# Kernel optimization log

Hardware: AMD Instinct MI355X
Metric: run time of the kernel (lower is better)

## Reference

```python
import jax, jax.numpy as jnp
import numpy as np

DIM = 256; H = 64; W = 64; NH = 8; NL = 1; NP = 8; HD = DIM // NH
B = 4


def _bilinear(img, grid):
    """torch.grid_sample(mode='bilinear', padding='zeros', align_corners=False).
    img: [C, Hl, Wl]; grid: [N, P, 2] normalized xy in [-1, 1]. Returns [C, N, P]."""
    Hl, Wl = img.shape[1], img.shape[2]
    x = (grid[..., 0] + 1.0) * (Wl * 0.5) - 0.5
    y = (grid[..., 1] + 1.0) * (Hl * 0.5) - 0.5
    x0 = jnp.floor(x); y0 = jnp.floor(y)
    wx = x - x0; wy = y - y0

    def gather(xi, yi):
        valid = (xi >= 0) & (xi < Wl) & (yi >= 0) & (yi < Hl)
        xc = jnp.clip(xi, 0, Wl - 1).astype(jnp.int32)
        yc = jnp.clip(yi, 0, Hl - 1).astype(jnp.int32)
        return img[:, yc, xc] * valid.astype(img.dtype)[None]  # [C, N, P]

    v00 = gather(x0, y0); v01 = gather(x0 + 1, y0)
    v10 = gather(x0, y0 + 1); v11 = gather(x0 + 1, y0 + 1)
    top = v00 * (1.0 - wx) + v01 * wx
    bot = v10 * (1.0 - wx) + v11 * wx
    return top * (1.0 - wy) + bot * wy


def _msda(value, loc, att):
    """multi_scale_deformable_attn_pytorch.
    value: [b, nv, NH, HD]; loc: [b, nq, NH, NL, NP, 2] in [0,1]; att: [b, nq, NH, NL, NP]."""
    b, nv, _, _ = value.shape
    nq = loc.shape[1]
    grids = 2.0 * loc - 1.0
    bn = b * NH
    level_shapes = [(H, W)] * NL  # all levels share the single [H, W] grid here
    sampled_levels = []
    offset = 0
    for l, (Hl, Wl) in enumerate(level_shapes):
        vl = value[:, offset:offset + Hl * Wl]                     # [b, HW, NH, HD]
        offset += Hl * Wl
        vl = vl.transpose(0, 2, 3, 1).reshape(bn, HD, Hl, Wl)      # [b*NH, HD, Hl, Wl]
        gl = grids[:, :, :, l].transpose(0, 2, 1, 3, 4).reshape(bn, nq, NP, 2)
        sampled_levels.append(jax.vmap(_bilinear)(vl, gl))         # [b*NH, HD, nq, NP]
    sampled = jnp.stack(sampled_levels, axis=3)                    # [b*NH, HD, nq, NL, NP]
    w = att.transpose(0, 2, 1, 3, 4).reshape(bn, 1, nq, NL, NP)
    out = jnp.sum(sampled * w, axis=(3, 4))                        # [b*NH, HD, nq]
    return out.reshape(b, NH, HD, nq).transpose(0, 3, 1, 2).reshape(b, nq, NH * HD)


def _forward(query, value, W_loc, b_loc, W_att, b_att, W_val, b_val, W_out, b_out):
    b = query.shape[0]
    nq = H * W
    q = query.transpose(0, 2, 3, 1).reshape(b, nq, DIM)
    v = value.transpose(0, 2, 3, 1).reshape(b, nq, DIM)
    loc = (q @ W_loc.T + b_loc).reshape(b, nq, NH, NL, NP, 2)
    att = jax.nn.softmax((q @ W_att.T + b_att).reshape(b, nq, NH, NL * NP), axis=-1)
    att = att.reshape(b, nq, NH, NL, NP)
    v = (v @ W_val.T + b_val).reshape(b, nq, NH, HD)
    out = _msda(v, loc, att)                                       # [b, nq, DIM]
    return out @ W_out.T + b_out


def setup_inputs() -> dict:
    key = jax.random.key(0)
    ks = jax.random.split(key, 12)
    s = 0.02
    return {
        "query": jax.random.normal(ks[0], (B, DIM, H, W), jnp.float32),
        "value": jax.random.normal(ks[1], (B, DIM, H, W), jnp.float32),
        "W_loc": jax.random.normal(ks[2], (NH * NL * NP * 2, DIM), jnp.float32) * s,
        "b_loc": jax.random.normal(ks[3], (NH * NL * NP * 2,), jnp.float32) * s,
        "W_att": jax.random.normal(ks[4], (NH * NL * NP, DIM), jnp.float32) * s,
        "b_att": jax.random.normal(ks[5], (NH * NL * NP,), jnp.float32) * s,
        "W_val": jax.random.normal(ks[6], (DIM, DIM), jnp.float32) * s,
        "b_val": jax.random.normal(ks[7], (DIM,), jnp.float32) * s,
        "W_out": jax.random.normal(ks[8], (DIM, DIM), jnp.float32) * s,
        "b_out": jax.random.normal(ks[9], (DIM,), jnp.float32) * s,
    }


def reference(query, value, W_loc, b_loc, W_att, b_att, W_val, b_val, W_out, b_out):
    return _forward(query, value, W_loc, b_loc, W_att, b_att, W_val, b_val, W_out, b_out)
```

## Files before the change

kernel.cpp:

```cpp
#include <hip/hip_runtime.h>
#include <hip/hip_bf16.h>
#include <math.h>

#define NQ   4096
#define DIMC 256
#define NHC  8
#define NPC  8
#define HDC  32
#define HC   64
#define WC   64
#define BC   4
#define KSTR 264

typedef __bf16 bf16x8 __attribute__((ext_vector_type(8)));
typedef __attribute__((ext_vector_type(4))) float f4;
typedef __attribute__((ext_vector_type(8))) short s8v;

__device__ __forceinline__ ushort f2bf(float f) {
  __hip_bfloat16 h = __float2bfloat16(f);
  union { __hip_bfloat16 h; ushort u; } c; c.h = h; return c.u;
}
__device__ __forceinline__ float bfu2f(ushort u) {
  union { unsigned i; float f; } c; c.i = ((unsigned)u) << 16; return c.f;
}
__device__ __forceinline__ float bflo(unsigned u) {
  union { unsigned i; float f; } c; c.i = u << 16; return c.f;
}
__device__ __forceinline__ float bfhi(unsigned u) {
  union { unsigned i; float f; } c; c.i = u & 0xffff0000u; return c.f;
}

union bfr8 { ushort u[8]; bf16x8 v; s8v s; };

__global__ __launch_bounds__(256) void k_proj(
    const float* __restrict__ query, const float* __restrict__ value,
    const float* __restrict__ W_loc, const float* __restrict__ b_loc,
    const float* __restrict__ W_att, const float* __restrict__ b_att,
    const float* __restrict__ W_val, const float* __restrict__ b_val,
    float* __restrict__ loc, float* __restrict__ att,
    ushort* __restrict__ vproj) {
  __shared__ __align__(16) ushort smem[2 * 64 * KSTR];
  const int tid = threadIdx.x;
  const int b = blockIdx.z, n0 = blockIdx.x * 64;
  const int lane = tid & 63, wid = tid >> 6;
  const int am = lane & 15, kq = (lane >> 4) * 8;
  const int row4 = (lane >> 4) * 4;
  const int an = tid & 63, ak = (tid >> 6) * 8;

  if (blockIdx.y == 0) {
    ushort* Ah = smem;
    ushort* Al = smem + 64 * KSTR;
    const float* Xb = query + (size_t)b * DIMC * NQ + n0 + an;
    for (int t = 0; t < 8; ++t) {
      const int kb = t * 32 + ak;
      float x[8];
#pragma unroll
      for (int j = 0; j < 8; ++j) x[j] = Xb[(size_t)(kb + j) * NQ];
      bfr8 ph, pl;
#pragma unroll
      for (int j = 0; j < 8; ++j) {
        ushort h = f2bf(x[j]);
        ph.u[j] = h;
        pl.u[j] = f2bf(x[j] - bfu2f(h));
      }
      *(s8v*)(&Ah[an * KSTR + kb]) = ph.s;
      *(s8v*)(&Al[an * KSTR + kb]) = pl.s;
    }
    __syncthreads();

    const int o0w = wid * 48;
    const float* Wr[3];
#pragma unroll
    for (int oj = 0; oj < 3; ++oj) {
      const int o = o0w + oj * 16 + am;
      Wr[oj] = (o < 128) ? (W_loc + (size_t)o * DIMC)
                         : (W_att + (size_t)(o - 128) * DIMC);
    }
    f4 acc[4][3];
#pragma unroll
    for (int mi = 0; mi < 4; ++mi)
#pragma unroll
      for (int oj = 0; oj < 3; ++oj) acc[mi][oj] = (f4)0.f;

#pragma unroll
    for (int t = 0; t < 8; ++t) {
      const int kk = t * 32 + kq;
      bf16x8 ah[4], al[4];
#pragma unroll
      for (int mi = 0; mi < 4; ++mi) {
        ah[mi] = *(const bf16x8*)(&Ah[(mi * 16 + am) * KSTR + kk]);
        al[mi] = *(const bf16x8*)(&Al[(mi * 16 + am) * KSTR + kk]);
      }
#pragma unroll
      for (int oj = 0; oj < 3; ++oj) {
        const float4 w0 = *(const float4*)(Wr[oj] + kk);
        const float4 w1 = *(const float4*)(Wr[oj] + kk + 4);
        const float wt[8] = {w0.x, w0.y, w0.z, w0.w, w1.x, w1.y, w1.z, w1.w};
        bfr8 bh, bl;
#pragma unroll
        for (int j = 0; j < 8; ++j) {
          ushort h = f2bf(wt[j]);
          bh.u[j] = h;
          bl.u[j] = f2bf(wt[j] - bfu2f(h));
        }
#pragma unroll
        for (int mi = 0; mi < 4; ++mi) {
          acc[mi][oj] = __builtin_amdgcn_mfma_f32_16x16x32_bf16(ah[mi], bh.v, acc[mi][oj], 0, 0, 0);
          acc[mi][oj] = __builtin_amdgcn_mfma_f32_16x16x32_bf16(al[mi], bh.v, acc[mi][oj], 0, 0, 0);
          acc[mi][oj] = __builtin_amdgcn_mfma_f32_16x16x32_bf16(ah[mi], bl.v, acc[mi][oj], 0, 0, 0);
        }
      }
    }
#pragma unroll
    for (int oj = 0; oj < 3; ++oj) {
      const int oA = o0w + oj * 16;
      const bool isAtt = (oA >= 128);
      float* dstBase = isAtt ? att : loc;
      const float* bias = isAtt ? b_att : b_loc;
      const int ostride = isAtt ? 64 : 128;
      const int o = (isAtt ? oA - 128 : oA) + am;
      const float bv = bias[o];
#pragma unroll
      for (int mi = 0; mi < 4; ++mi) {
        const int nb = n0 + mi * 16 + row4;
#pragma unroll
        for (int r = 0; r < 4; ++r)
          dstBase[((size_t)b * NQ + nb + r) * ostride + o] = acc[mi][oj][r] + bv;
      }
    }
  } else {
    ushort* As = smem;
    const float* Xb = value + (size_t)b * DIMC * NQ + n0 + an;
    for (int t = 0; t < 8; ++t) {
      const int kb = t * 32 + ak;
      float x[8];
#pragma unroll
      for (int j = 0; j < 8; ++j) x[j] = Xb[(size_t)(kb + j) * NQ];
      bfr8 pa;
#pragma unroll
      for (int j = 0; j < 8; ++j) pa.u[j] = f2bf(x[j]);
      *(s8v*)(&As[an * KSTR + kb]) = pa.s;
    }
    __syncthreads();

    const int o0w = wid * 64;
    const float* Wr[4];
#pragma unroll
    for (int oj = 0; oj < 4; ++oj)
      Wr[oj] = W_val + (size_t)(o0w + oj * 16 + am) * DIMC;

    f4 acc[4][4];
#pragma unroll
    for (int mi = 0; mi < 4; ++mi)
#pragma unroll
      for (int oj = 0; oj < 4; ++oj) acc[mi][oj] = (f4)0.f;

#pragma unroll
    for (int t = 0; t < 8; ++t) {
      const int kk = t * 32 + kq;
      bf16x8 af[4];
#pragma unroll
      for (int mi = 0; mi < 4; ++mi)
        af[mi] = *(const bf16x8*)(&As[(mi * 16 + am) * KSTR + kk]);
#pragma unroll
      for (int oj = 0; oj < 4; ++oj) {
        const float4 w0 = *(const float4*)(Wr[oj] + kk);
        const float4 w1 = *(const float4*)(Wr[oj] + kk + 4);
        const float wt[8] = {w0.x, w0.y, w0.z, w0.w, w1.x, w1.y, w1.z, w1.w};
        bfr8 bh;
#pragma unroll
        for (int j = 0; j < 8; ++j) bh.u[j] = f2bf(wt[j]);
#pragma unroll
        for (int mi = 0; mi < 4; ++mi)
          acc[mi][oj] = __builtin_amdgcn_mfma_f32_16x16x32_bf16(af[mi], bh.v, acc[mi][oj], 0, 0, 0);
      }
    }
#pragma unroll
    for (int oj = 0; oj < 4; ++oj) {
      const int o = o0w + oj * 16 + am;
      const int h = o >> 5, d = o & 31;
      const float bias = b_val[o];
      ushort* dst = vproj + ((size_t)(b * NHC + h) * NQ) * HDC + d;
#pragma unroll
      for (int mi = 0; mi < 4; ++mi) {
        const int nb = n0 + mi * 16 + row4;
#pragma unroll
        for (int r = 0; r < 4; ++r)
          dst[(size_t)(nb + r) * HDC] = f2bf(acc[mi][oj][r] + bias);
      }
    }
  }
}

__global__ __launch_bounds__(256) void k_sample(
    const float* __restrict__ loc, const float* __restrict__ attL,
    const ushort* __restrict__ vproj, ushort* __restrict__ msda) {
  __shared__ float4 Lc[64][9];
  __shared__ int4   Lo[64][9];
  const int b = blockIdx.z, h = blockIdx.y;
  const int tid = threadIdx.x;
  const int n0 = blockIdx.x * 64;
#pragma unroll
  for (int it = 0; it < 2; ++it) {
    const int idx = it * 256 + tid;
    const int q = idx >> 3, p = idx & 7;
    const int n = n0 + q;
    const float lg = attL[((size_t)b * NQ + n) * 64 + h * 8 + p];
    float m = lg;
#pragma unroll
    for (int off = 1; off < 8; off <<= 1) m = fmaxf(m, __shfl_xor(m, off, 64));
    const float e = __expf(lg - m);
    float s = e;
#pragma unroll
    for (int off = 1; off < 8; off <<= 1) s += __shfl_xor(s, off, 64);
    const float w = e / s;
    const float2 xy = *(const float2*)(loc + ((size_t)b * NQ + n) * 128 + h * 16 + p * 2);
    const float x = xy.x * 64.0f - 0.5f;
    const float y = xy.y * 64.0f - 0.5f;
    const float x0f = floorf(x), y0f = floorf(y);
    const float wx = x - x0f, wy = y - y0f;
    const int x0 = (int)x0f, y0 = (int)y0f;
    const int x1 = x0 + 1, y1 = y0 + 1;
    const float fx0 = (x0 >= 0 && x0 < WC) ? 1.f : 0.f;
    const float fx1 = (x1 >= 0 && x1 < WC) ? 1.f : 0.f;
    const float fy0 = (y0 >= 0 && y0 < HC) ? 1.f : 0.f;
    const float fy1 = (y1 >= 0 && y1 < HC) ? 1.f : 0.f;
    const int cx0 = min(max(x0, 0), WC - 1), cx1 = min(max(x1, 0), WC - 1);
    const int cy0 = min(max(y0, 0), HC - 1), cy1 = min(max(y1, 0), HC - 1);
    float4 cf;
    cf.x = w * (1.f - wx) * (1.f - wy) * fx0 * fy0;
    cf.y = w * wx * (1.f - wy) * fx1 * fy0;
    cf.z = w * (1.f - wx) * wy * fx0 * fy1;
    cf.w = w * wx * wy * fx1 * fy1;
    int4 of;
    of.x = (cy0 * WC + cx0) * HDC; of.y = (cy0 * WC + cx1) * HDC;
    of.z = (cy1 * WC + cx0) * HDC; of.w = (cy1 * WC + cx1) * HDC;
    Lc[q][p] = cf; Lo[q][p] = of;
  }
  __syncthreads();
  const int q = tid >> 2, d8 = (tid & 3) * 8;
  const int n = n0 + q;
  const ushort* vb = vproj + (size_t)((b * NHC + h) * NQ) * HDC + d8;
  float a[8] = {};
#pragma unroll
  for (int p = 0; p < 8; ++p) {
    const int4 of = Lo[q][p];
    const float4 cf = Lc[q][p];
    const uint4 u00 = *(const uint4*)(vb + of.x);
    const uint4 u01 = *(const uint4*)(vb + of.y);
    const uint4 u10 = *(const uint4*)(vb + of.z);
    const uint4 u11 = *(const uint4*)(vb + of.w);
    const unsigned c00[4] = {u00.x, u00.y, u00.z, u00.w};
    const unsigned c01[4] = {u01.x, u01.y, u01.z, u01.w};
    const unsigned c10[4] = {u10.x, u10.y, u10.z, u10.w};
    const unsigned c11[4] = {u11.x, u11.y, u11.z, u11.w};
#pragma unroll
    for (int j = 0; j < 4; ++j) {
      a[2 * j]     += cf.x * bflo(c00[j]) + cf.y * bflo(c01[j]) + cf.z * bflo(c10[j]) + cf.w * bflo(c11[j]);
      a[2 * j + 1] += cf.x * bfhi(c00[j]) + cf.y * bfhi(c01[j]) + cf.z * bfhi(c10[j]) + cf.w * bfhi(c11[j]);
    }
  }
  bfr8 r;
#pragma unroll
  for (int j = 0; j < 8; ++j) r.u[j] = f2bf(a[j]);
  *(s8v*)(msda + ((size_t)b * NQ + n) * DIMC + h * HDC + d8) = r.s;
}

__global__ __launch_bounds__(256) void k_out(
    const ushort* __restrict__ msda, const float* __restrict__ W_out,
    const float* __restrict__ b_out, float* __restrict__ out) {
  __shared__ __align__(16) ushort As[64 * KSTR];
  const int b = blockIdx.z, n0 = blockIdx.x * 64;
  const int tid = threadIdx.x, lane = tid & 63, wid = tid >> 6;
  const int am = lane & 15, kq = (lane >> 4) * 8;
  const int row4 = (lane >> 4) * 4;

  const int an = tid >> 2, akc = (tid & 3) * 64;
  const ushort* Ap = msda + ((size_t)b * NQ + n0 + an) * DIMC + akc;
  s8v av[8];
#pragma unroll
  for (int j = 0; j < 8; ++j) av[j] = *(const s8v*)(Ap + j * 8);
#pragma unroll
  for (int j = 0; j < 8; ++j) *(s8v*)(&As[an * KSTR + akc + j * 8]) = av[j];
  __syncthreads();

  const int o0w = wid * 64;
  const float* Wr[4];
#pragma unroll
  for (int oj = 0; oj < 4; ++oj)
    Wr[oj] = W_out + (size_t)(o0w + oj * 16 + am) * DIMC;

  f4 acc[4][4];
#pragma unroll
  for (int mi = 0; mi < 4; ++mi)
#pragma unroll
    for (int oj = 0; oj < 4; ++oj) acc[mi][oj] = (f4)0.f;

#pragma unroll
  for (int t = 0; t < 8; ++t) {
    const int kk = t * 32 + kq;
    bf16x8 af[4];
#pragma unroll
    for (int mi = 0; mi < 4; ++mi)
      af[mi] = *(const bf16x8*)(&As[(mi * 16 + am) * KSTR + kk]);
#pragma unroll
    for (int oj = 0; oj < 4; ++oj) {
      const float4 w0 = *(const float4*)(Wr[oj] + kk);
      const float4 w1 = *(const float4*)(Wr[oj] + kk + 4);
      const float wt[8] = {w0.x, w0.y, w0.z, w0.w, w1.x, w1.y, w1.z, w1.w};
      bfr8 bh;
#pragma unroll
      for (int j = 0; j < 8; ++j) bh.u[j] = f2bf(wt[j]);
#pragma unroll
      for (int mi = 0; mi < 4; ++mi)
        acc[mi][oj] = __builtin_amdgcn_mfma_f32_16x16x32_bf16(af[mi], bh.v, acc[mi][oj], 0, 0, 0);
    }
  }
#pragma unroll
  for (int oj = 0; oj < 4; ++oj) {
    const int o = o0w + oj * 16 + am;
    const float bias = b_out[o];
#pragma unroll
    for (int mi = 0; mi < 4; ++mi) {
      const int nb = n0 + mi * 16 + row4;
#pragma unroll
      for (int r = 0; r < 4; ++r)
        out[((size_t)b * NQ + nb + r) * DIMC + o] = acc[mi][oj][r] + bias;
    }
  }
}

extern "C" void kernel_launch(void* const* d_in, const int* in_sizes, int n_in,
                              void* d_out, int out_size, void* d_ws, size_t ws_size,
                              hipStream_t stream) {
  const float* query = (const float*)d_in[0];
  const float* value = (const float*)d_in[1];
  const float* W_loc = (const float*)d_in[2];
  const float* b_loc = (const float*)d_in[3];
  const float* W_att = (const float*)d_in[4];
  const float* b_att = (const float*)d_in[5];
  const float* W_val = (const float*)d_in[6];
  const float* b_val = (const float*)d_in[7];
  const float* W_out = (const float*)d_in[8];
  const float* b_out = (const float*)d_in[9];
  float* out = (float*)d_out;

  float* ws = (float*)d_ws;
  float* loc    = ws;
  float* att    = loc + (size_t)BC * NQ * 128;
  ushort* vproj = (ushort*)(att + (size_t)BC * NQ * 64);
  ushort* msda  = vproj + (size_t)BC * NHC * NQ * HDC;

  dim3 blk(256);
  k_proj  <<<dim3(NQ / 64, 2, BC), blk, 0, stream>>>(query, value, W_loc, b_loc,
             W_att, b_att, W_val, b_val, loc, att, vproj);
  k_sample<<<dim3(NQ / 64, NHC, BC), blk, 0, stream>>>(loc, att, vproj, msda);
  k_out   <<<dim3(NQ / 64, 1, BC), blk, 0, stream>>>(msda, W_out, b_out, out);
}
```

Before: 148.6 us.

## Stage weights in LDS with K-chunked register-prefetch pipeline and smaller row tiles

Both GEMM kernels (k_proj and k_out) now tile the K dimension in chunks of 32. Each chunk's weight slice is converted to bf16 once per block and stored in shared memory, instead of every wave re-reading and re-converting weights from global memory. The next chunk's activations and weights are prefetched into registers while the current chunk is computed. The row tile drops from 64 to 32, which doubles the grid and cuts LDS use, trading more weight traffic across blocks for better occupancy and more parallelism. Two barriers per K step are added.

```diff
diff --git a/kernel.cpp b/kernel.cpp
--- a/kernel.cpp
+++ b/kernel.cpp
@@ -10,7 +10,7 @@
 #define HC   64
 #define WC   64
 #define BC   4
-#define KSTR 264
+#define WSTR 40
 
 typedef __bf16 bf16x8 __attribute__((ext_vector_type(8)));
 typedef __attribute__((ext_vector_type(4))) float f4;
@@ -39,75 +39,95 @@
     const float* __restrict__ W_val, const float* __restrict__ b_val,
     float* __restrict__ loc, float* __restrict__ att,
     ushort* __restrict__ vproj) {
-  __shared__ __align__(16) ushort smem[2 * 64 * KSTR];
-  const int tid = threadIdx.x;
-  const int b = blockIdx.z, n0 = blockIdx.x * 64;
+  __shared__ __align__(16) ushort smem[17920];
+  const int tid = threadIdx.x, b = blockIdx.z, n0 = blockIdx.x * 32;
   const int lane = tid & 63, wid = tid >> 6;
-  const int am = lane & 15, kq = (lane >> 4) * 8;
-  const int row4 = (lane >> 4) * 4;
-  const int an = tid & 63, ak = (tid >> 6) * 8;
+  const int am = lane & 15, kq = (lane >> 4) * 8, row4 = (lane >> 4) * 4;
+  const int an = tid & 31, akg = (tid >> 5) * 4;
 
   if (blockIdx.y == 0) {
     ushort* Ah = smem;
-    ushort* Al = smem + 64 * KSTR;
+    ushort* Al = smem + 1280;
+    ushort* Wh = smem + 2560;
+    ushort* Wl = smem + 10240;
     const float* Xb = query + (size_t)b * DIMC * NQ + n0 + an;
+    int crow[3], ckp[3];
+    const float* Wr[3];
+#pragma unroll
+    for (int i = 0; i < 3; ++i) {
+      const int cc = tid * 3 + i;
+      crow[i] = cc >> 2; ckp[i] = (cc & 3) * 8;
+      Wr[i] = ((crow[i] < 128) ? (W_loc + (size_t)crow[i] * DIMC)
+                               : (W_att + (size_t)(crow[i] - 128) * DIMC)) + ckp[i];
+    }
+    float ax[4];
+    float4 wp[3][2];
+#pragma unroll
+    for (int j = 0; j < 4; ++j) ax[j] = Xb[(size_t)(akg + j) * NQ];
+#pragma unroll
+    for (int i = 0; i < 3; ++i) {
+      wp[i][0] = *(const float4*)(Wr[i]);
+      wp[i][1] = *(const float4*)(Wr[i] + 4);
+    }
+    const int o0w = wid * 48;
+    f4 acc[2][3];
+#pragma unroll
+    for (int mi = 0; mi < 2; ++mi)
+#pragma unroll
+      for (int oj = 0; oj < 3; ++oj) acc[mi][oj] = (f4)0.f;
+
     for (int t = 0; t < 8; ++t) {
-      const int kb = t * 32 + ak;
-      float x[8];
-#pragma unroll
-      for (int j = 0; j < 8; ++j) x[j] = Xb[(size_t)(kb + j) * NQ];
-      bfr8 ph, pl;
-#pragma unroll
-      for (int j = 0; j < 8; ++j) {
-        ushort h = f2bf(x[j]);
-        ph.u[j] = h;
-        pl.u[j] = f2bf(x[j] - bfu2f(h));
-      }
-      *(s8v*)(&Ah[an * KSTR + kb]) = ph.s;
-      *(s8v*)(&Al[an * KSTR + kb]) = pl.s;
-    }
-    __syncthreads();
-
-    const int o0w = wid * 48;
-    const float* Wr[3];
-#pragma unroll
-    for (int oj = 0; oj < 3; ++oj) {
-      const int o = o0w + oj * 16 + am;
-      Wr[oj] = (o < 128) ? (W_loc + (size_t)o * DIMC)
-                         : (W_att + (size_t)(o - 128) * DIMC);
-    }
-    f4 acc[4][3];
-#pragma unroll
-    for (int mi = 0; mi < 4; ++mi)
-#pragma unroll
-      for (int oj = 0; oj < 3; ++oj) acc[mi][oj] = (f4)0.f;
-
-#pragma unroll
-    for (int t = 0; t < 8; ++t) {
-      const int kk = t * 32 + kq;
-      bf16x8 ah[4], al[4];
-#pragma unroll
-      for (int mi = 0; mi < 4; ++mi) {
-        ah[mi] = *(const bf16x8*)(&Ah[(mi * 16 + am) * KSTR + kk]);
-        al[mi] = *(const bf16x8*)(&Al[(mi * 16 + am) * KSTR + kk]);
+      __syncthreads();
+      {
+        ushort4 hh, ll;
+        float a0 = ax[0], a1 = ax[1], a2 = ax[2], a3 = ax[3];
+        hh.x = f2bf(a0); ll.x = f2bf(a0 - bfu2f(hh.x));
+        hh.y = f2bf(a1); ll.y = f2bf(a1 - bfu2f(hh.y));
+        hh.z = f2bf(a2); ll.z = f2bf(a2 - bfu2f(hh.z));
+        hh.w = f2bf(a3); ll.w = f2bf(a3 - bfu2f(hh.w));
+        *(ushort4*)(&Ah[an * WSTR + akg]) = hh;
+        *(ushort4*)(&Al[an * WSTR + akg]) = ll;
+#pragma unroll
+        for (int i = 0; i < 3; ++i) {
+          const float wt[8] = {wp[i][0].x, wp[i][0].y, wp[i][0].z, wp[i][0].w,
+                               wp[i][1].x, wp[i][1].y, wp[i][1].z, wp[i][1].w};
+          bfr8 bh, bl;
+#pragma unroll
+          for (int j = 0; j < 8; ++j) {
+            ushort h = f2bf(wt[j]);
+            bh.u[j] = h;
+            bl.u[j] = f2bf(wt[j] - bfu2f(h));
+          }
+          *(s8v*)(&Wh[crow[i] * WSTR + ckp[i]]) = bh.s;
+          *(s8v*)(&Wl[crow[i] * WSTR + ckp[i]]) = bl.s;
+        }
+      }
+      if (t < 7) {
+        const int k0 = (t + 1) * 32;
+#pragma unroll
+        for (int j = 0; j < 4; ++j) ax[j] = Xb[(size_t)(k0 + akg + j) * NQ];
+#pragma unroll
+        for (int i = 0; i < 3; ++i) {
+          wp[i][0] = *(const float4*)(Wr[i] + k0);
+          wp[i][1] = *(const float4*)(Wr[i] + k0 + 4);
+        }
+      }
+      __syncthreads();
+      bf16x8 ah[2], al[2];
+#pragma unroll
+      for (int mi = 0; mi < 2; ++mi) {
+        ah[mi] = *(const bf16x8*)(&Ah[(mi * 16 + am) * WSTR + kq]);
+        al[mi] = *(const bf16x8*)(&Al[(mi * 16 + am) * WSTR + kq]);
       }
 #pragma unroll
       for (int oj = 0; oj < 3; ++oj) {
-        const float4 w0 = *(const float4*)(Wr[oj] + kk);
-        const float4 w1 = *(const float4*)(Wr[oj] + kk + 4);
-        const float wt[8] = {w0.x, w0.y, w0.z, w0.w, w1.x, w1.y, w1.z, w1.w};
-        bfr8 bh, bl;
-#pragma unroll
-        for (int j = 0; j < 8; ++j) {
-          ushort h = f2bf(wt[j]);
-          bh.u[j] = h;
-          bl.u[j] = f2bf(wt[j] - bfu2f(h));
-        }
-#pragma unroll
-        for (int mi = 0; mi < 4; ++mi) {
-          acc[mi][oj] = __builtin_amdgcn_mfma_f32_16x16x32_bf16(ah[mi], bh.v, acc[mi][oj], 0, 0, 0);
-          acc[mi][oj] = __builtin_amdgcn_mfma_f32_16x16x32_bf16(al[mi], bh.v, acc[mi][oj], 0, 0, 0);
-          acc[mi][oj] = __builtin_amdgcn_mfma_f32_16x16x32_bf16(ah[mi], bl.v, acc[mi][oj], 0, 0, 0);
+        bf16x8 bh = *(const bf16x8*)(&Wh[(o0w + oj * 16 + am) * WSTR + kq]);
+        bf16x8 bl = *(const bf16x8*)(&Wl[(o0w + oj * 16 + am) * WSTR + kq]);
+#pragma unroll
+        for (int mi = 0; mi < 2; ++mi) {
+          acc[mi][oj] = __builtin_amdgcn_mfma_f32_16x16x32_bf16(ah[mi], bh, acc[mi][oj], 0, 0, 0);
+          acc[mi][oj] = __builtin_amdgcn_mfma_f32_16x16x32_bf16(al[mi], bh, acc[mi][oj], 0, 0, 0);
+          acc[mi][oj] = __builtin_amdgcn_mfma_f32_16x16x32_bf16(ah[mi], bl, acc[mi][oj], 0, 0, 0);
         }
       }
     }
@@ -121,7 +141,7 @@
       const int o = (isAtt ? oA - 128 : oA) + am;
       const float bv = bias[o];
 #pragma unroll
-      for (int mi = 0; mi < 4; ++mi) {
+      for (int mi = 0; mi < 2; ++mi) {
         const int nb = n0 + mi * 16 + row4;
 #pragma unroll
         for (int r = 0; r < 4; ++r)
@@ -130,49 +150,64 @@
     }
   } else {
     ushort* As = smem;
+    ushort* Ws = smem + 2560;
     const float* Xb = value + (size_t)b * DIMC * NQ + n0 + an;
+    const float* Wr = W_val + (size_t)tid * DIMC;
+
+    float ax[4];
+    float4 wp[4][2];
+#pragma unroll
+    for (int j = 0; j < 4; ++j) ax[j] = Xb[(size_t)(akg + j) * NQ];
+#pragma unroll
+    for (int c = 0; c < 4; ++c) {
+      wp[c][0] = *(const float4*)(Wr + c * 8);
+      wp[c][1] = *(const float4*)(Wr + c * 8 + 4);
+    }
+    const int o0w = wid * 64;
+    f4 acc[2][4];
+#pragma unroll
+    for (int mi = 0; mi < 2; ++mi)
+#pragma unroll
+      for (int oj = 0; oj < 4; ++oj) acc[mi][oj] = (f4)0.f;
+
     for (int t = 0; t < 8; ++t) {
-      const int kb = t * 32 + ak;
-      float x[8];
-#pragma unroll
-      for (int j = 0; j < 8; ++j) x[j] = Xb[(size_t)(kb + j) * NQ];
-      bfr8 pa;
-#pragma unroll
-      for (int j = 0; j < 8; ++j) pa.u[j] = f2bf(x[j]);
-      *(s8v*)(&As[an * KSTR + kb]) = pa.s;
-    }
-    __syncthreads();
-
-    const int o0w = wid * 64;
-    const float* Wr[4];
-#pragma unroll
-    for (int oj = 0; oj < 4; ++oj)
-      Wr[oj] = W_val + (size_t)(o0w + oj * 16 + am) * DIMC;
-
-    f4 acc[4][4];
-#pragma unroll
-    for (int mi = 0; mi < 4; ++mi)
-#pragma unroll
-      for (int oj = 0; oj < 4; ++oj) acc[mi][oj] = (f4)0.f;
-
-#pragma unroll
-    for (int t = 0; t < 8; ++t) {
-      const int kk = t * 32 + kq;
-      bf16x8 af[4];
-#pragma unroll
-      for (int mi = 0; mi < 4; ++mi)
-        af[mi] = *(const bf16x8*)(&As[(mi * 16 + am) * KSTR + kk]);
+      __syncthreads();
+      {
+        ushort4 hh;
+        hh.x = f2bf(ax[0]); hh.y = f2bf(ax[1]);
+        hh.z = f2bf(ax[2]); hh.w = f2bf(ax[3]);
+        *(ushort4*)(&As[an * WSTR + akg]) = hh;
+#pragma unroll
+        for (int c = 0; c < 4; ++c) {
+          const float wt[8] = {wp[c][0].x, wp[c][0].y, wp[c][0].z, wp[c][0].w,
+                               wp[c][1].x, wp[c][1].y, wp[c][1].z, wp[c][1].w};
+          bfr8 bh;
+#pragma unroll
+          for (int j = 0; j < 8; ++j) bh.u[j] = f2bf(wt[j]);
+          *(s8v*)(&Ws[tid * WSTR + c * 8]) = bh.s;
+        }
+      }
+      if (t < 7) {
+        const int k0 = (t + 1) * 32;
+#pragma unroll
+        for (int j = 0; j < 4; ++j) ax[j] = Xb[(size_t)(k0 + akg + j) * NQ];
+#pragma unroll
+        for (int c = 0; c < 4; ++c) {
+          wp[c][0] = *(const float4*)(Wr + k0 + c * 8);
+          wp[c][1] = *(const float4*)(Wr + k0 + c * 8 + 4);
+        }
+      }
+      __syncthreads();
+      bf16x8 af[2];
+#pragma unroll
+      for (int mi = 0; mi < 2; ++mi)
+        af[mi] = *(const bf16x8*)(&As[(mi * 16 + am) * WSTR + kq]);
 #pragma unroll
       for (int oj = 0; oj < 4; ++oj) {
-        const float4 w0 = *(const float4*)(Wr[oj] + kk);
-        const float4 w1 = *(const float4*)(Wr[oj] + kk + 4);
-        const float wt[8] = {w0.x, w0.y, w0.z, w0.w, w1.x, w1.y, w1.z, w1.w};
-        bfr8 bh;
-#pragma unroll
-        for (int j = 0; j < 8; ++j) bh.u[j] = f2bf(wt[j]);
-#pragma unroll
-        for (int mi = 0; mi < 4; ++mi)
-          acc[mi][oj] = __builtin_amdgcn_mfma_f32_16x16x32_bf16(af[mi], bh.v, acc[mi][oj], 0, 0, 0);
+        bf16x8 bf = *(const bf16x8*)(&Ws[(o0w + oj * 16 + am) * WSTR + kq]);
+#pragma unroll
+        for (int mi = 0; mi < 2; ++mi)
+          acc[mi][oj] = __builtin_amdgcn_mfma_f32_16x16x32_bf16(af[mi], bf, acc[mi][oj], 0, 0, 0);
       }
     }
 #pragma unroll
@@ -182,7 +217,7 @@
       const float bias = b_val[o];
       ushort* dst = vproj + ((size_t)(b * NHC + h) * NQ) * HDC + d;
 #pragma unroll
-      for (int mi = 0; mi < 4; ++mi) {
+      for (int mi = 0; mi < 2; ++mi) {
         const int nb = n0 + mi * 16 + row4;
 #pragma unroll
         for (int r = 0; r < 4; ++r)
@@ -269,51 +304,64 @@
 __global__ __launch_bounds__(256) void k_out(
     const ushort* __restrict__ msda, const float* __restrict__ W_out,
     const float* __restrict__ b_out, float* __restrict__ out) {
-  __shared__ __align__(16) ushort As[64 * KSTR];
-  const int b = blockIdx.z, n0 = blockIdx.x * 64;
-  const int tid = threadIdx.x, lane = tid & 63, wid = tid >> 6;
-  const int am = lane & 15, kq = (lane >> 4) * 8;
-  const int row4 = (lane >> 4) * 4;
-
-  const int an = tid >> 2, akc = (tid & 3) * 64;
-  const ushort* Ap = msda + ((size_t)b * NQ + n0 + an) * DIMC + akc;
-  s8v av[8];
-#pragma unroll
-  for (int j = 0; j < 8; ++j) av[j] = *(const s8v*)(Ap + j * 8);
-#pragma unroll
-  for (int j = 0; j < 8; ++j) *(s8v*)(&As[an * KSTR + akc + j * 8]) = av[j];
-  __syncthreads();
-
+  __shared__ __align__(16) ushort smem[11520];
+  ushort* As = smem;
+  ushort* Ws = smem + 1280;
+  const int tid = threadIdx.x, b = blockIdx.z, n0 = blockIdx.x * 32;
+  const int lane = tid & 63, wid = tid >> 6;
+  const int am = lane & 15, kq = (lane >> 4) * 8, row4 = (lane >> 4) * 4;
+
+  const int an = tid & 31, akh = ((tid >> 5) & 3) * 8;
+  const ushort* Ap = msda + ((size_t)b * NQ + n0 + an) * DIMC + akh;
+  const float* Wr = W_out + (size_t)tid * DIMC;
+
+  s8v av = {};
+  if (tid < 128) av = *(const s8v*)(Ap);
+  float4 wp[4][2];
+#pragma unroll
+  for (int c = 0; c < 4; ++c) {
+    wp[c][0] = *(const float4*)(Wr + c * 8);
+    wp[c][1] = *(const float4*)(Wr + c * 8 + 4);
+  }
   const int o0w = wid * 64;
-  const float* Wr[4];
-#pragma unroll
-  for (int oj = 0; oj < 4; ++oj)
-    Wr[oj] = W_out + (size_t)(o0w + oj * 16 + am) * DIMC;
-
-  f4 acc[4][4];
-#pragma unroll
-  for (int mi = 0; mi < 4; ++mi)
+  f4 acc[2][4];
+#pragma unroll
+  for (int mi = 0; mi < 2; ++mi)
 #pragma unroll
     for (int oj = 0; oj < 4; ++oj) acc[mi][oj] = (f4)0.f;
 
-#pragma unroll
   for (int t = 0; t < 8; ++t) {
-    const int kk = t * 32 + kq;
-    bf16x8 af[4];
-#pragma unroll
-    for (int mi = 0; mi < 4; ++mi)
-      af[mi] = *(const bf16x8*)(&As[(mi * 16 + am) * KSTR + kk]);
+    __syncthreads();
+    if (tid < 128) *(s8v*)(&As[an * WSTR + akh]) = av;
+#pragma unroll
+    for (int c = 0; c < 4; ++c) {
+      const float wt[8] = {wp[c][0].x, wp[c][0].y, wp[c][0].z, wp[c][0].w,
+                           wp[c][1].x, wp[c][1].y, wp[c][1].z, wp[c][1].w};
+      bfr8 bh;
+#pragma unroll
+      for (int j = 0; j < 8; ++j) bh.u[j] = f2bf(wt[j]);
+      *(s8v*)(&Ws[tid * WSTR + c * 8]) = bh.s;
+    }
+    if (t < 7) {
+      const int k0 = (t + 1) * 32;
+      if (tid < 128) av = *(const s8v*)(Ap + k0);
+#pragma unroll
+      for (int c = 0; c < 4; ++c) {
+        wp[c][0] = *(const float4*)(Wr + k0 + c * 8);
+        wp[c][1] = *(const float4*)(Wr + k0 + c * 8 + 4);
+      }
+    }
+    __syncthreads();
+    bf16x8 af[2];
+#pragma unroll
+    for (int mi = 0; mi < 2; ++mi)
+      af[mi] = *(const bf16x8*)(&As[(mi * 16 + am) * WSTR + kq]);
 #pragma unroll
     for (int oj = 0; oj < 4; ++oj) {
-      const float4 w0 = *(const float4*)(Wr[oj] + kk);
-      const float4 w1 = *(const float4*)(Wr[oj] + kk + 4);
-      const float wt[8] = {w0.x, w0.y, w0.z, w0.w, w1.x, w1.y, w1.z, w1.w};
-      bfr8 bh;
-#pragma unroll
-      for (int j = 0; j < 8; ++j) bh.u[j] = f2bf(wt[j]);
-#pragma unroll
-      for (int mi = 0; mi < 4; ++mi)
-        acc[mi][oj] = __builtin_amdgcn_mfma_f32_16x16x32_bf16(af[mi], bh.v, acc[mi][oj], 0, 0, 0);
+      bf16x8 bf = *(const bf16x8*)(&Ws[(o0w + oj * 16 + am) * WSTR + kq]);
+#pragma unroll
+      for (int mi = 0; mi < 2; ++mi)
+        acc[mi][oj] = __builtin_amdgcn_mfma_f32_16x16x32_bf16(af[mi], bf, acc[mi][oj], 0, 0, 0);
     }
   }
 #pragma unroll
@@ -321,7 +369,7 @@
     const int o = o0w + oj * 16 + am;
     const float bias = b_out[o];
 #pragma unroll
-    for (int mi = 0; mi < 4; ++mi) {
+    for (int mi = 0; mi < 2; ++mi) {
       const int nb = n0 + mi * 16 + row4;
 #pragma unroll
       for (int r = 0; r < 4; ++r)
@@ -352,8 +400,8 @@
   ushort* msda  = vproj + (size_t)BC * NHC * NQ * HDC;
 
   dim3 blk(256);
-  k_proj  <<<dim3(NQ / 64, 2, BC), blk, 0, stream>>>(query, value, W_loc, b_loc,
+  k_proj  <<<dim3(NQ / 32, 2, BC), blk, 0, stream>>>(query, value, W_loc, b_loc,
              W_att, b_att, W_val, b_val, loc, att, vproj);
   k_sample<<<dim3(NQ / 64, NHC, BC), blk, 0, stream>>>(loc, att, vproj, msda);
-  k_out   <<<dim3(NQ / 64, 1, BC), blk, 0, stream>>>(msda, W_out, b_out, out);
-}
+  k_out   <<<dim3(NQ / 32, 1, BC), blk, 0, stream>>>(msda, W_out, b_out, out);
+}
```

Result: slower. 159.2 us (+7.2%).
